# Performance work log

Hardware: AMD Instinct MI355X
Metric: run time of the kernel (lower is better)

Reference implementation:

```python
import jax, jax.numpy as jnp
from jax import lax
import numpy as np

CH = 16
STAGES = 6
DN = ('NDHWC', 'DHWIO', 'NDHWC')


def setup_inputs() -> dict:
    key = jax.random.key(0)
    ks = jax.random.split(key, 16)
    B, G = 8, 64
    x = jax.random.normal(ks[0], (B, G, G, G, 1), dtype=jnp.float32)
    mask = jax.random.randint(ks[1], (B, G, G, G), 0, 2, dtype=jnp.int32)
    meta = jax.random.normal(ks[2], (B, 3), dtype=jnp.float32)
    sched = jax.random.normal(ks[3], (B, 128), dtype=jnp.float32)
    s = 0.05
    w_stem = jax.random.normal(ks[4], (5, 5, 5, 1, CH), dtype=jnp.float32) * s
    w_stages = jax.random.normal(ks[5], (STAGES, 3, 3, 3, CH, CH), dtype=jnp.float32) * s
    meta_w1 = jax.random.normal(ks[6], (3, 32), dtype=jnp.float32) * s
    meta_b1 = jnp.zeros((32,), jnp.float32)
    meta_w2 = jax.random.normal(ks[7], (32, 16), dtype=jnp.float32) * s
    meta_b2 = jnp.zeros((16,), jnp.float32)
    mat_w = jax.random.normal(ks[8], (CH * STAGES + 16, 128), dtype=jnp.float32) * s
    mat_b = jnp.zeros((128,), jnp.float32)
    sch_w = jax.random.normal(ks[9], (128, 128), dtype=jnp.float32) * s
    sch_b = jnp.zeros((128,), jnp.float32)
    f1_w = jax.random.normal(ks[10], (256, 128), dtype=jnp.float32) * s
    f1_b = jnp.zeros((128,), jnp.float32)
    f2_w = jax.random.normal(ks[11], (128, 1), dtype=jnp.float32) * s
    f2_b = jnp.zeros((1,), jnp.float32)
    return dict(x=x, mask=mask, meta=meta, sched=sched, w_stem=w_stem,
                w_stages=w_stages, meta_w1=meta_w1, meta_b1=meta_b1,
                meta_w2=meta_w2, meta_b2=meta_b2, mat_w=mat_w, mat_b=mat_b,
                sch_w=sch_w, sch_b=sch_b, f1_w=f1_w, f1_b=f1_b,
                f2_w=f2_w, f2_b=f2_b)


def _pool_mask(m):
    # ME stride-2 output coords = unique(coords // 2): 2x2x2 max-pool, ceil sizes
    return lax.reduce_window(m, jnp.float32(0), lax.max,
                             (1, 2, 2, 2), (1, 2, 2, 2), 'SAME')


def reference(x, mask, meta, sched, w_stem, w_stages, meta_w1, meta_b1,
              meta_w2, meta_b2, mat_w, mat_b, sch_w, sch_b,
              f1_w, f1_b, f2_w, f2_b):
    m = mask.astype(x.dtype)
    feats = x * m[..., None]                       # zero features off-mask
    y = lax.conv_general_dilated(feats, w_stem, (1, 1, 1), 'SAME',
                                 dimension_numbers=DN)
    y = jnp.maximum(y * m[..., None], 0.0)         # stem: conv + mask + ReLU
    pools = []
    for i in range(STAGES):
        y = lax.conv_general_dilated(y, w_stages[i], (2, 2, 2),
                                     [(1, 1), (1, 1), (1, 1)],
                                     dimension_numbers=DN)
        m = _pool_mask(m)
        y = jnp.maximum(y * m[..., None], 0.0)
        denom = jnp.maximum(m.sum(axis=(1, 2, 3)), 1.0)   # occupied voxels
        pools.append(y.sum(axis=(1, 2, 3)) / denom[:, None])
    pools = jnp.concatenate(pools, axis=1)                 # [B, CH*STAGES]
    h = jax.nn.relu(meta[:, :3] @ meta_w1 + meta_b1)
    meta_emb = h @ meta_w2 + meta_b2                        # [B,16]
    m_emb = jax.nn.relu(jnp.concatenate([pools, meta_emb], 1) @ mat_w + mat_b)
    s_emb = jax.nn.relu(sched @ sch_w + sch_b)
    z = jnp.concatenate([m_emb, s_emb], axis=1)             # [B,256]
    z = jax.nn.relu(z @ f1_w + f1_b)
    return z @ f2_w + f2_b                                  # [B,1]
```

## Files before the change

### kernel.cpp

```cpp
#include <hip/hip_runtime.h>

#define CH 16
#define NB 8

typedef unsigned short u16;
typedef unsigned int u32;
typedef __attribute__((ext_vector_type(8))) short s16x8;
typedef __attribute__((ext_vector_type(4))) float f32x4;

__device__ __forceinline__ float bflo(u32 u) { return __uint_as_float(u << 16); }
__device__ __forceinline__ float bfhi(u32 u) { return __uint_as_float(u & 0xffff0000u); }
__device__ __forceinline__ u32 bfrnd(float f) {
  u32 u = __float_as_uint(f);
  return (u + 0x7fffu + ((u >> 16) & 1u)) >> 16;
}
__device__ __forceinline__ u32 packbf(float lo, float hi) {
  return bfrnd(lo) | (bfrnd(hi) << 16);
}

__global__ __launch_bounds__(256) void bprep_kernel(
    const float* __restrict__ w_stg, const float* __restrict__ w_stem,
    u16* __restrict__ bpre)
{
  const int e = blockIdx.x * 256 + (int)threadIdx.x;
  if (e >= 4 * 7168 + 3584) return;
  if (e < 4 * 7168) {
    const int s = e / 7168, r0 = e % 7168;
    const int i = r0 >> 9;
    const int r = r0 & 511;
    const int l = r >> 3, j = r & 7;
    const int tap = 2 * i + (l >> 5);
    const int cin = ((l >> 4) & 1) * 8 + j;
    const int n = l & 15;
    const float* w = w_stg + s * 27 * 256;
    const float val = (tap < 27) ? w[(tap * 16 + cin) * 16 + n] : 0.f;
    bpre[s * 7168 + i * 512 + l * 8 + j] = (u16)bfrnd(val);
  } else {
    const int e2 = e - 4 * 7168;
    const int i = e2 >> 9;
    const int r0 = e2 & 511;
    const int lane = r0 >> 3, j = r0 & 7;
    const int quad = lane >> 4, n = lane & 15;
    const int r = i * 4 + quad;
    const float val = (r < 25 && j < 5) ? w_stem[(r * 5 + j) * 16 + n] : 0.f;
    bpre[4 * 7168 + e2] = (u16)bfrnd(val);
  }
}

__global__ __launch_bounds__(256) void stem_mfma(
    const float* __restrict__ x, const int* __restrict__ mask,
    const u16* __restrict__ bpre, u16* __restrict__ yout,
    float* __restrict__ pool_sum, float* __restrict__ cnt)
{
  __shared__ u16 tl[144 * 24];
  __shared__ u16 cp[8 * 1168];

  const int b = blockIdx.y;
  const int u = blockIdx.x;
  const int tb = ((u & 7) << 6) | (u >> 3);
  const int z0 = (tb >> 6) * 8;
  const int y0 = ((tb >> 3) & 7) * 8;
  const int x0 = (tb & 7) * 8;
  const int tid = threadIdx.x;

  if (tb == 0) {
    if (tid < 96) pool_sum[b * 96 + tid] = 0.f;
    else if (tid < 102) cnt[b * 6 + (tid - 96)] = 0.f;
  }

  const int lane = tid & 63;
  const int wv = tid >> 6;
  const int n = lane & 15;
  const int quad = lane >> 4;
  const int vy = n >> 2, vx = n & 3;

  s16x8 wf[7];
  {
    const s16x8* wfp = (const s16x8*)(bpre + 4 * 7168);
#pragma unroll
    for (int i = 0; i < 7; ++i) wf[i] = wfp[i * 64 + lane];
  }

  for (int i = tid; i < 1728; i += 256) {
    const int row = i / 12;
    const int lx = i - row * 12;
    const int lz = row / 12;
    const int ly = row - lz * 12;
    const int gz = z0 + lz - 2, gy = y0 + ly - 2, gx = x0 + lx - 2;
    float v = 0.f;
    if ((unsigned)gz < 64u && (unsigned)gy < 64u && (unsigned)gx < 64u) {
      const int gi = ((b * 64 + gz) * 64 + gy) * 64 + gx;
      v = x[gi] * (float)mask[gi];
    }
    tl[row * 24 + lx] = (u16)bfrnd(v);
  }
  __syncthreads();

  if (tid < 144) {
    const uint4 a = *(const uint4*)&tl[tid * 24];
    const uint2 bq = *(const uint2*)&tl[tid * 24 + 8];
    u32 c[7];
    c[0] = a.x; c[1] = a.y; c[2] = a.z; c[3] = a.w;
    c[4] = bq.x; c[5] = bq.y; c[6] = 0u;
    u32 d[7];
#pragma unroll
    for (int k = 0; k < 6; ++k) d[k] = (c[k] >> 16) | (c[k + 1] << 16);
    d[6] = c[6] >> 16;
    uint4* dst = (uint4*)&cp[tid * 8];
    dst[0 * 146] = make_uint4(c[0], c[1], c[2], c[3]);
    dst[1 * 146] = make_uint4(d[0], d[1], d[2], d[3]);
    dst[2 * 146] = make_uint4(c[1], c[2], c[3], c[4]);
    dst[3 * 146] = make_uint4(d[1], d[2], d[3], d[4]);
    dst[4 * 146] = make_uint4(c[2], c[3], c[4], c[5]);
    dst[5 * 146] = make_uint4(d[2], d[3], d[4], d[5]);
    dst[6 * 146] = make_uint4(c[3], c[4], c[5], c[6]);
    dst[7 * 146] = make_uint4(d[3], d[4], d[5], d[6]);
  }
  __syncthreads();

  int doff[7];
#pragma unroll
  for (int i = 0; i < 7; ++i) {
    const int r = i * 4 + quad;
    doff[i] = (r < 25) ? ((r / 5) * 12 + (r % 5)) * 8 : 0;
  }

  for (int s = 0; s < 8; ++s) {
    const int sz = (s >> 2) * 4, sy = ((s >> 1) & 1) * 4, sx = (s & 1) * 4;
    const int base =
        (sx + vx) * 1168 + (((sz + wv) * 12) + (sy + vy)) * 8;
    f32x4 acc = {0.f, 0.f, 0.f, 0.f};
#pragma unroll
    for (int i = 0; i < 7; ++i) {
      const s16x8 bf = *(const s16x8*)&cp[base + doff[i]];
      acc = __builtin_amdgcn_mfma_f32_16x16x32_bf16(wf[i], bf, acc, 0, 0, 0);
    }
    const int Z = z0 + sz + wv, Y = y0 + sy + vy, X = x0 + sx + vx;
    const int gi = ((b * 64 + Z) * 64 + Y) * 64 + X;
    const float mv = (float)mask[gi];
    const float f0 = fmaxf(acc[0], 0.f) * mv;
    const float f1 = fmaxf(acc[1], 0.f) * mv;
    const float f2 = fmaxf(acc[2], 0.f) * mv;
    const float f3 = fmaxf(acc[3], 0.f) * mv;
    uint2* op = (uint2*)(yout + (size_t)gi * CH + quad * 4);
    op[0] = make_uint2(packbf(f0, f1), packbf(f2, f3));
  }
}

template <int S>
__global__ __launch_bounds__(256) void stage_mfma4(
    const u16* __restrict__ yin, const u16* __restrict__ bpre,
    const int* __restrict__ m_in_i, const float* __restrict__ m_in_f,
    u16* __restrict__ yout, float* __restrict__ m_out,
    float* __restrict__ pool_sum, float* __restrict__ cnt,
    const int stage)
{
  __shared__ u16 lb[14 * 512];
  __shared__ float lC[4 * 16 * 17];
  __shared__ float lmp[256];

  constexpr int So = S >> 1;
  constexpr int nvox = So * So * So;
  const int b = blockIdx.y;
  const int tid = threadIdx.x;
  const int vg0 = blockIdx.x * 256;

  {
    const uint4* src = (const uint4*)bpre;
    uint4* dst = (uint4*)lb;
    for (int e = tid; e < 896; e += 256) dst[e] = src[e];
  }

  {
    const int vox = vg0 + tid;
    const int oz = vox / (So * So);
    const int oy = (vox / So) % So;
    const int ox = vox % So;
    float mp = 0.f;
#pragma unroll
    for (int dz = 0; dz < 2; ++dz)
#pragma unroll
      for (int dy = 0; dy < 2; ++dy)
#pragma unroll
        for (int dx = 0; dx < 2; ++dx) {
          const int mi =
              ((b * S + 2 * oz + dz) * S + 2 * oy + dy) * S + 2 * ox + dx;
          const float mv = m_in_i ? (float)m_in_i[mi] : m_in_f[mi];
          mp = fmaxf(mp, mv);
        }
    lmp[tid] = mp;
  }
  __syncthreads();

  const int wv = tid >> 6;
  const int lane = tid & 63;
  const int m = lane & 15;
  const int quad = lane >> 4;
  const int qh = quad >> 1;
  const int qlo = quad & 1;

  int izb[4], iyb[4], ixb[4];
#pragma unroll
  for (int g = 0; g < 4; ++g) {
    const int vox = vg0 + wv * 64 + g * 16 + m;
    const int oz = vox / (So * So);
    const int oy = (vox / So) % So;
    const int ox = vox % So;
    izb[g] = 2 * oz - 1;
    iyb[g] = 2 * oy - 1;
    ixb[g] = 2 * ox - 1;
  }

  const s16x8* lbv = (const s16x8*)lb;
  f32x4 acc[4];
#pragma unroll
  for (int g = 0; g < 4; ++g) acc[g] = (f32x4){0.f, 0.f, 0.f, 0.f};

#pragma unroll
  for (int i = 0; i < 14; ++i) {
    const int t0 = 2 * i, t1 = 2 * i + 1;
    const int dz0 = t0 / 9, dy0 = (t0 / 3) % 3, dx0 = t0 % 3;
    const int dz1 = (t1 < 27) ? t1 / 9 : 1;
    const int dy1 = (t1 < 27) ? (t1 / 3) % 3 : 1;
    const int dx1 = (t1 < 27) ? t1 % 3 : 1;
    const int dzq = qh ? dz1 : dz0;
    const int dyq = qh ? dy1 : dy0;
    const int dxq = qh ? dx1 : dx0;

    uint4 ar[4];
#pragma unroll
    for (int g = 0; g < 4; ++g) {
      const int iz = izb[g] + dzq;
      const int iy = iyb[g] + dyq;
      const int ix = ixb[g] + dxq;
      const bool valid = (unsigned)iz < (unsigned)S &&
                         (unsigned)iy < (unsigned)S &&
                         (unsigned)ix < (unsigned)S;
      const int izc = min(max(iz, 0), S - 1);
      const int iyc = min(max(iy, 0), S - 1);
      const int ixc = min(max(ix, 0), S - 1);
      const size_t addr =
          (size_t)(((b * S + izc) * S + iyc) * S + ixc) * 16 + qlo * 8;
      uint4 v = *(const uint4*)(yin + addr);
      v.x = valid ? v.x : 0u;
      v.y = valid ? v.y : 0u;
      v.z = valid ? v.z : 0u;
      v.w = valid ? v.w : 0u;
      ar[g] = v;
    }
    const s16x8 bfrag = lbv[i * 64 + lane];
#pragma unroll
    for (int g = 0; g < 4; ++g)
      acc[g] = __builtin_amdgcn_mfma_f32_16x16x32_bf16(
          __builtin_bit_cast(s16x8, ar[g]), bfrag, acc[g], 0, 0, 0);
  }

  float psum = 0.f;
#pragma unroll
  for (int g = 0; g < 4; ++g) {
    __syncthreads();
    {
      float* lCw = lC + wv * 272;
      const int n = lane & 15;
#pragma unroll
      for (int reg = 0; reg < 4; ++reg) {
        const int row = quad * 4 + reg;
        lCw[row * 17 + n] =
            fmaxf(acc[g][reg], 0.f) * lmp[wv * 64 + g * 16 + row];
      }
    }
    __syncthreads();
    {
      const int vox_l = tid >> 2;
      const int cg = (tid & 3) * 4;
      const float* src = lC + (vox_l >> 4) * 272 + (vox_l & 15) * 17 + cg;
      const float f0 = src[0], f1 = src[1], f2 = src[2], f3 = src[3];
      const int lv = (vox_l >> 4) * 64 + g * 16 + (vox_l & 15);
      const size_t gi = (size_t)b * nvox + vg0 + lv;
      uint2* op = (uint2*)(yout + gi * 16 + cg);
      op[0] = make_uint2(packbf(f0, f1), packbf(f2, f3));
      if ((tid & 3) == 0) m_out[gi] = lmp[lv];
    }
    if (tid < 16) {
      float s = 0.f;
#pragma unroll 16
      for (int v = 0; v < 64; ++v)
        s += lC[(v >> 4) * 272 + (v & 15) * 17 + tid];
      psum += s;
    }
  }
  if (tid < 16) {
    atomicAdd(&pool_sum[(b * 6 + stage) * 16 + tid], psum);
  } else if (tid == 16) {
    float c = 0.f;
#pragma unroll 16
    for (int v = 0; v < 256; ++v) c += lmp[v];
    atomicAdd(&cnt[b * 6 + stage], c);
  }
}

__global__ __launch_bounds__(256) void tail_kernel(
    const u16* __restrict__ y3g, const float* __restrict__ m3g,
    const u16* __restrict__ bpre,
    const float* __restrict__ wstg,
    const float* __restrict__ meta, const float* __restrict__ sched,
    const float* __restrict__ mw1, const float* __restrict__ mb1,
    const float* __restrict__ mw2, const float* __restrict__ mb2,
    const float* __restrict__ matw, const float* __restrict__ matb,
    const float* __restrict__ schw, const float* __restrict__ schb,
    const float* __restrict__ f1w, const float* __restrict__ f1b,
    const float* __restrict__ f2w, const float* __restrict__ f2b,
    const float* __restrict__ pool_sum, const float* __restrict__ cnt,
    float* __restrict__ out)
{
  const int b = blockIdx.x;
  const int t = threadIdx.x;
  __shared__ u16 ty3[8192];
  __shared__ float lm3[512];
  __shared__ float pb[4 * 64 * 17];
  __shared__ float ly4[64 * 16];
  __shared__ float lm4[64];
  __shared__ float ps4[256];
  __shared__ float ly5[8 * 16];
  __shared__ float lm5[8];
  __shared__ float ps5[128];
  __shared__ float lsum[3][16];
  __shared__ float lcnt[3];
  __shared__ float invec[112];
  __shared__ float hbuf[32];
  __shared__ float zbuf[256];
  __shared__ float psf[256];
  __shared__ float part[2];

  {
    const uint4* yb = (const uint4*)(y3g + (size_t)b * 8192);
    uint4* dst = (uint4*)ty3;
    for (int i = t; i < 1024; i += 256) dst[i] = yb[i];
    for (int i = t; i < 512; i += 256) lm3[i] = m3g[b * 512 + i];
  }
  __syncthreads();

  {
    const int lane = t & 63;
    const int wv = t >> 6;
    const int mm = lane & 15;
    const int quad = lane >> 4;
    const int qh = quad >> 1, qlo = quad & 1;

    int iz0[4], iy0[4], ix0[4];
#pragma unroll
    for (int g = 0; g < 4; ++g) {
      const int vox = g * 16 + mm;
      iz0[g] = 2 * (vox >> 4) - 1;
      iy0[g] = 2 * ((vox >> 2) & 3) - 1;
      ix0[g] = 2 * (vox & 3) - 1;
    }
    f32x4 a3[4];
#pragma unroll
    for (int g = 0; g < 4; ++g) a3[g] = (f32x4){0.f, 0.f, 0.f, 0.f};
    const s16x8* bp3 = (const s16x8*)(bpre + 3 * 7168);
#pragma unroll
    for (int ii = 0; ii < 4; ++ii) {
      const int i = wv * 4 + ii;
      if (i < 14) {
        const int t0 = 2 * i, t1 = 2 * i + 1;
        const int dz0 = t0 / 9, dy0 = (t0 / 3) % 3, dx0 = t0 % 3;
        const int dz1 = (t1 < 27) ? t1 / 9 : 1;
        const int dy1 = (t1 < 27) ? (t1 / 3) % 3 : 1;
        const int dx1 = (t1 < 27) ? t1 % 3 : 1;
        const int dzq = qh ? dz1 : dz0;
        const int dyq = qh ? dy1 : dy0;
        const int dxq = qh ? dx1 : dx0;
        uint4 ar[4];
#pragma unroll
        for (int g = 0; g < 4; ++g) {
          const int iz = iz0[g] + dzq;
          const int iy = iy0[g] + dyq;
          const int ix = ix0[g] + dxq;
          const bool valid = (unsigned)iz < 8u && (unsigned)iy < 8u &&
                             (unsigned)ix < 8u;
          const int izc = min(max(iz, 0), 7);
          const int iyc = min(max(iy, 0), 7);
          const int ixc = min(max(ix, 0), 7);
          const int ad = ((izc * 8 + iyc) * 8 + ixc) * 16 + qlo * 8;
          uint4 v = *(const uint4*)&ty3[ad];
          v.x = valid ? v.x : 0u;
          v.y = valid ? v.y : 0u;
          v.z = valid ? v.z : 0u;
          v.w = valid ? v.w : 0u;
          ar[g] = v;
        }
        const s16x8 bf = bp3[i * 64 + lane];
#pragma unroll
        for (int g = 0; g < 4; ++g)
          a3[g] = __builtin_amdgcn_mfma_f32_16x16x32_bf16(
              __builtin_bit_cast(s16x8, ar[g]), bf, a3[g], 0, 0, 0);
      }
    }
#pragma unroll
    for (int g = 0; g < 4; ++g)
#pragma unroll
      for (int reg = 0; reg < 4; ++reg)
        pb[wv * 1088 + (g * 16 + quad * 4 + reg) * 17 + mm] = a3[g][reg];
  }
  __syncthreads();

  {
    const int vox = t >> 2, cg = (t & 3) * 4;
    const int oz = vox >> 4, oy = (vox >> 2) & 3, ox = vox & 3;
    float mp = 0.f;
#pragma unroll
    for (int dz = 0; dz < 2; ++dz)
#pragma unroll
      for (int dy = 0; dy < 2; ++dy)
#pragma unroll
        for (int dx = 0; dx < 2; ++dx)
          mp = fmaxf(mp, lm3[((2 * oz + dz) * 8 + 2 * oy + dy) * 8 +
                             2 * ox + dx]);
#pragma unroll
    for (int c = 0; c < 4; ++c) {
      const int ch = cg + c;
      const float s = pb[vox * 17 + ch] + pb[1088 + vox * 17 + ch] +
                      pb[2176 + vox * 17 + ch] + pb[3264 + vox * 17 + ch];
      ly4[vox * 16 + ch] = fmaxf(s, 0.f) * mp;
    }
    if (cg == 0) lm4[vox] = mp;
  }
  __syncthreads();

  if (t < 16) {
    float s = 0.f;
#pragma unroll 16
    for (int v = 0; v < 64; ++v) s += ly4[v * 16 + t];
    lsum[0][t] = s;
  } else if (t == 16) {
    float s = 0.f;
#pragma unroll 16
    for (int v = 0; v < 64; ++v) s += lm4[v];
    lcnt[0] = s;
  }
  {
    const float* w = wstg + 4 * 27 * 256;
    const int o = t >> 1, kh = t & 1;
    const int vox4 = o >> 4, co = o & 15;
    const int oz = vox4 >> 2, oy = (vox4 >> 1) & 1, ox = vox4 & 1;
    float acc = 0.f;
#pragma unroll
    for (int tt = 0; tt < 14; ++tt) {
      const int tap = tt + (kh ? 14 : 0);
      if (tap < 27) {
        const int dz = tap / 9, dy = (tap / 3) % 3, dx = tap % 3;
        const int iz = 2 * oz + dz - 1, iy = 2 * oy + dy - 1,
                  ix = 2 * ox + dx - 1;
        const float s = ((unsigned)iz < 4u && (unsigned)iy < 4u &&
                         (unsigned)ix < 4u) ? 1.f : 0.f;
        const int idx = ((min(max(iz, 0), 3) * 4 + min(max(iy, 0), 3)) * 4 +
                         min(max(ix, 0), 3)) * 16;
        const float* wp = w + tap * 256 + co;
#pragma unroll
        for (int ci = 0; ci < 16; ++ci)
          acc = fmaf(ly4[idx + ci] * s, wp[ci * 16], acc);
      }
    }
    ps4[t] = acc;
  }
  __syncthreads();

  if (t < 128) {
    const int vox4 = t >> 4, co = t & 15;
    float mp = 0.f;
#pragma unroll
    for (int dz = 0; dz < 2; ++dz)
#pragma unroll
      for (int dy = 0; dy < 2; ++dy)
#pragma unroll
        for (int dx = 0; dx < 2; ++dx)
          mp = fmaxf(mp, lm4[((2 * (vox4 >> 2) + dz) * 4 +
                              2 * ((vox4 >> 1) & 1) + dy) * 4 +
                             2 * (vox4 & 1) + dx]);
    ly5[t] = fmaxf(ps4[2 * t] + ps4[2 * t + 1], 0.f) * mp;
    if (co == 0) lm5[vox4] = mp;
  }
  __syncthreads();

  if (t < 16) {
    float s = 0.f;
#pragma unroll
    for (int v = 0; v < 8; ++v) s += ly5[v * 16 + t];
    lsum[1][t] = s;
  } else if (t == 16) {
    lcnt[1] = lm5[0] + lm5[1] + lm5[2] + lm5[3] + lm5[4] + lm5[5] + lm5[6] +
              lm5[7];
  }
  if (t < 128) {
    const float* w = wstg + 5 * 27 * 256;
    const int co = t & 15, k8 = t >> 4;
    float acc = 0.f;
#pragma unroll
    for (int tt = 0; tt < 4; ++tt) {
      const int tap = k8 * 4 + tt;
      if (tap < 27) {
        const int dz = tap / 9, dy = (tap / 3) % 3, dx = tap % 3;
        const int iz = dz - 1, iy = dy - 1, ix = dx - 1;
        const float s = ((unsigned)iz < 2u && (unsigned)iy < 2u &&
                         (unsigned)ix < 2u) ? 1.f : 0.f;
        const int idx = ((min(max(iz, 0), 1) * 2 + min(max(iy, 0), 1)) * 2 +
                         min(max(ix, 0), 1)) * 16;
        const float* wp = w + tap * 256 + co;
#pragma unroll
        for (int ci = 0; ci < 16; ++ci)
          acc = fmaf(ly5[idx + ci] * s, wp[ci * 16], acc);
      }
    }
    ps5[t] = acc;
  }
  __syncthreads();

  if (t < 16) {
    float s = ps5[t] + ps5[16 + t] + ps5[32 + t] + ps5[48 + t] +
              ps5[64 + t] + ps5[80 + t] + ps5[96 + t] + ps5[112 + t];
    float mp = 0.f;
#pragma unroll
    for (int v = 0; v < 8; ++v) mp = fmaxf(mp, lm5[v]);
    lsum[2][t] = fmaxf(s, 0.f) * mp;
    if (t == 0) lcnt[2] = mp;
  } else if (t >= 96 && t < 128) {
    const int j = t - 96;
    float h = mb1[j];
#pragma unroll
    for (int k = 0; k < 3; ++k) h = fmaf(meta[b * 3 + k], mw1[k * 32 + j], h);
    hbuf[j] = fmaxf(h, 0.f);
  }
  __syncthreads();

  if (t < 48) {
    const int s = t >> 4;
    invec[t] = pool_sum[b * 96 + t] / fmaxf(cnt[b * 6 + s], 1.f);
  } else if (t < 96) {
    const int s = (t >> 4) - 3;
    invec[t] = lsum[s][t & 15] / fmaxf(lcnt[s], 1.f);
  } else if (t < 112) {
    const int j = t - 96;
    float e = mb2[j];
#pragma unroll
    for (int k = 0; k < 32; ++k) e = fmaf(hbuf[k], mw2[k * 16 + j], e);
    invec[t] = e;
  }
  __syncthreads();

  if (t < 128) {
    float a = matb[t];
#pragma unroll 16
    for (int k = 0; k < 112; ++k) a = fmaf(invec[k], matw[k * 128 + t], a);
    zbuf[t] = fmaxf(a, 0.f);
  } else {
    const int c = t - 128;
    float s = schb[c];
#pragma unroll 16
    for (int k = 0; k < 128; ++k)
      s = fmaf(sched[b * 128 + k], schw[k * 128 + c], s);
    zbuf[128 + c] = fmaxf(s, 0.f);
  }
  __syncthreads();

  {
    const int col = t & 127, kh = t >> 7;
    float a = 0.f;
#pragma unroll 16
    for (int kk = 0; kk < 128; ++kk) {
      const int k = kh * 128 + kk;
      a = fmaf(zbuf[k], f1w[k * 128 + col], a);
    }
    psf[t] = a;
  }
  __syncthreads();

  if (t < 128) {
    const float a = psf[t] + psf[128 + t] + f1b[t];
    float v = fmaxf(a, 0.f) * f2w[t];
#pragma unroll
    for (int off = 32; off > 0; off >>= 1) v += __shfl_xor(v, off, 64);
    if ((t & 63) == 0) part[t >> 6] = v;
  }
  __syncthreads();
  if (t == 0) out[b] = part[0] + part[1] + f2b[0];
}

extern "C" void kernel_launch(void* const* d_in, const int* in_sizes, int n_in,
                              void* d_out, int out_size, void* d_ws,
                              size_t ws_size, hipStream_t stream)
{
  (void)in_sizes; (void)n_in; (void)out_size; (void)ws_size;
  const float* x      = (const float*)d_in[0];
  const int*   mask   = (const int*)  d_in[1];
  const float* meta   = (const float*)d_in[2];
  const float* sched  = (const float*)d_in[3];
  const float* w_stem = (const float*)d_in[4];
  const float* w_stg  = (const float*)d_in[5];
  const float* mw1    = (const float*)d_in[6];
  const float* mb1    = (const float*)d_in[7];
  const float* mw2    = (const float*)d_in[8];
  const float* mb2    = (const float*)d_in[9];
  const float* matw   = (const float*)d_in[10];
  const float* matb   = (const float*)d_in[11];
  const float* schw   = (const float*)d_in[12];
  const float* schb   = (const float*)d_in[13];
  const float* f1w    = (const float*)d_in[14];
  const float* f1b    = (const float*)d_in[15];
  const float* f2w    = (const float*)d_in[16];
  const float* f2b    = (const float*)d_in[17];
  float* out = (float*)d_out;

  char* ws = (char*)d_ws;
  size_t off = 0;
  auto alloc = [&](size_t nbytes) -> void* {
    void* p = ws + off;
    off += (nbytes + 255) & ~(size_t)255;
    return p;
  };

  u16* y0 = (u16*)alloc((size_t)NB * 64 * 64 * 64 * CH * 2);
  u16* y1 = (u16*)alloc((size_t)NB * 32 * 32 * 32 * CH * 2);
  u16* y2 = (u16*)alloc((size_t)NB * 16 * 16 * 16 * CH * 2);
  u16* y3 = (u16*)alloc((size_t)NB * 8 * 8 * 8 * CH * 2);
  float* m1 = (float*)alloc((size_t)NB * 32 * 32 * 32 * 4);
  float* m2 = (float*)alloc((size_t)NB * 16 * 16 * 16 * 4);
  float* m3 = (float*)alloc((size_t)NB * 8 * 8 * 8 * 4);
  float* pool_sum = (float*)alloc((NB * 96 + NB * 6) * 4);
  float* cnt = pool_sum + NB * 96;
  u16* bpre = (u16*)alloc((4 * 7168 + 3584) * 2);

  bprep_kernel<<<126, 256, 0, stream>>>(w_stg, w_stem, bpre);

  stem_mfma<<<dim3(512, NB), 256, 0, stream>>>(x, mask, bpre, y0,
                                               pool_sum, cnt);

  stage_mfma4<64><<<dim3(128, NB), 256, 0, stream>>>(
      y0, bpre + 0 * 7168, mask, (const float*)nullptr, y1, m1,
      pool_sum, cnt, 0);
  stage_mfma4<32><<<dim3(16, NB), 256, 0, stream>>>(
      y1, bpre + 1 * 7168, (const int*)nullptr, m1, y2, m2,
      pool_sum, cnt, 1);
  stage_mfma4<16><<<dim3(2, NB), 256, 0, stream>>>(
      y2, bpre + 2 * 7168, (const int*)nullptr, m2, y3, m3,
      pool_sum, cnt, 2);

  tail_kernel<<<NB, 256, 0, stream>>>(y3, m3, bpre, w_stg, meta, sched,
                                      mw1, mb1, mw2, mb2, matw, matb,
                                      schw, schb, f1w, f1b, f2w, f2b,
                                      pool_sum, cnt, out);
}
```

Before: 203.8 us.

## Fuse stem input staging into direct vectorized row loads with hardware bf16 packing

The stem kernel no longer stages the masked input tile into an intermediate LDS buffer. Each of 144 threads now loads its 12-element x row and mask row with float2/int2 vector loads and builds the shifted bf16 pairs directly in registers. This removes one LDS pass and one barrier. The output mask value is prefetched one sub-block ahead, output addresses are precomputed, a v_cvt_pk_bf16_f32 instruction replaces the software bf16 round-and-pack, and an occupancy hint of 6 is added to launch bounds. Fewer threads now participate in the global loads, so latency hiding during the load phase may be reduced.

Measured after the change: 196.5 us. 1.04x faster.

```diff
diff --git a/kernel.cpp b/kernel.cpp
--- a/kernel.cpp
+++ b/kernel.cpp
@@ -14,8 +14,10 @@
   u32 u = __float_as_uint(f);
   return (u + 0x7fffu + ((u >> 16) & 1u)) >> 16;
 }
-__device__ __forceinline__ u32 packbf(float lo, float hi) {
-  return bfrnd(lo) | (bfrnd(hi) << 16);
+__device__ __forceinline__ u32 packbf_hw(float lo, float hi) {
+  u32 r;
+  asm("v_cvt_pk_bf16_f32 %0, %1, %2" : "=v"(r) : "v"(lo), "v"(hi));
+  return r;
 }
 
 __global__ __launch_bounds__(256) void bprep_kernel(
@@ -47,12 +49,11 @@
   }
 }
 
-__global__ __launch_bounds__(256) void stem_mfma(
+__global__ __launch_bounds__(256, 6) void stem_mfma(
     const float* __restrict__ x, const int* __restrict__ mask,
     const u16* __restrict__ bpre, u16* __restrict__ yout,
     float* __restrict__ pool_sum, float* __restrict__ cnt)
 {
-  __shared__ u16 tl[144 * 24];
   __shared__ u16 cp[8 * 1168];
 
   const int b = blockIdx.y;
@@ -81,40 +82,63 @@
     for (int i = 0; i < 7; ++i) wf[i] = wfp[i * 64 + lane];
   }
 
-  for (int i = tid; i < 1728; i += 256) {
-    const int row = i / 12;
-    const int lx = i - row * 12;
-    const int lz = row / 12;
-    const int ly = row - lz * 12;
-    const int gz = z0 + lz - 2, gy = y0 + ly - 2, gx = x0 + lx - 2;
-    float v = 0.f;
-    if ((unsigned)gz < 64u && (unsigned)gy < 64u && (unsigned)gx < 64u) {
-      const int gi = ((b * 64 + gz) * 64 + gy) * 64 + gx;
-      v = x[gi] * (float)mask[gi];
-    }
-    tl[row * 24 + lx] = (u16)bfrnd(v);
-  }
-  __syncthreads();
-
   if (tid < 144) {
-    const uint4 a = *(const uint4*)&tl[tid * 24];
-    const uint2 bq = *(const uint2*)&tl[tid * 24 + 8];
-    u32 c[7];
-    c[0] = a.x; c[1] = a.y; c[2] = a.z; c[3] = a.w;
-    c[4] = bq.x; c[5] = bq.y; c[6] = 0u;
-    u32 d[7];
-#pragma unroll
-    for (int k = 0; k < 6; ++k) d[k] = (c[k] >> 16) | (c[k + 1] << 16);
-    d[6] = c[6] >> 16;
+    const int lz = tid / 12, ly = tid - lz * 12;
+    const int gz = z0 + lz - 2, gy = y0 + ly - 2;
     uint4* dst = (uint4*)&cp[tid * 8];
-    dst[0 * 146] = make_uint4(c[0], c[1], c[2], c[3]);
-    dst[1 * 146] = make_uint4(d[0], d[1], d[2], d[3]);
-    dst[2 * 146] = make_uint4(c[1], c[2], c[3], c[4]);
-    dst[3 * 146] = make_uint4(d[1], d[2], d[3], d[4]);
-    dst[4 * 146] = make_uint4(c[2], c[3], c[4], c[5]);
-    dst[5 * 146] = make_uint4(d[2], d[3], d[4], d[5]);
-    dst[6 * 146] = make_uint4(c[3], c[4], c[5], c[6]);
-    dst[7 * 146] = make_uint4(d[3], d[4], d[5], d[6]);
+    if ((unsigned)gz < 64u && (unsigned)gy < 64u) {
+      const long long rowg =
+          ((long long)((b * 64 + gz) * 64 + gy)) * 64 + (x0 - 2);
+      float v[12];
+      if (rowg >= 0 && rowg + 12 <= (long long)NB * 64 * 64 * 64) {
+        const float2* xp = (const float2*)(x + rowg);
+        const int2* mp2 = (const int2*)(mask + rowg);
+        float2 xv[6]; int2 mv2[6];
+#pragma unroll
+        for (int j = 0; j < 6; ++j) { xv[j] = xp[j]; mv2[j] = mp2[j]; }
+#pragma unroll
+        for (int j = 0; j < 6; ++j) {
+          v[2 * j]     = xv[j].x * (float)mv2[j].x;
+          v[2 * j + 1] = xv[j].y * (float)mv2[j].y;
+        }
+        if (x0 == 0)  { v[0] = 0.f;  v[1] = 0.f;  }
+        if (x0 == 56) { v[10] = 0.f; v[11] = 0.f; }
+      } else {
+#pragma unroll
+        for (int j = 0; j < 12; ++j) {
+          const int gx = x0 - 2 + j;
+          float vv = 0.f;
+          if ((unsigned)gx < 64u) {
+            const long long gi = rowg + j;
+            vv = x[gi] * (float)mask[gi];
+          }
+          v[j] = vv;
+        }
+      }
+      const u32 c0 = packbf_hw(v[0], v[1]);
+      const u32 c1 = packbf_hw(v[2], v[3]);
+      const u32 c2 = packbf_hw(v[4], v[5]);
+      const u32 c3 = packbf_hw(v[6], v[7]);
+      const u32 c4 = packbf_hw(v[8], v[9]);
+      const u32 c5 = packbf_hw(v[10], v[11]);
+      const u32 d0 = packbf_hw(v[1], v[2]);
+      const u32 d1 = packbf_hw(v[3], v[4]);
+      const u32 d2 = packbf_hw(v[5], v[6]);
+      const u32 d3 = packbf_hw(v[7], v[8]);
+      const u32 d4 = packbf_hw(v[9], v[10]);
+      const u32 d5 = packbf_hw(v[11], 0.f);
+      dst[0 * 146] = make_uint4(c0, c1, c2, c3);
+      dst[1 * 146] = make_uint4(d0, d1, d2, d3);
+      dst[2 * 146] = make_uint4(c1, c2, c3, c4);
+      dst[3 * 146] = make_uint4(d1, d2, d3, d4);
+      dst[4 * 146] = make_uint4(c2, c3, c4, c5);
+      dst[5 * 146] = make_uint4(d2, d3, d4, d5);
+      dst[6 * 146] = make_uint4(c3, c4, c5, 0u);
+      dst[7 * 146] = make_uint4(d3, d4, d5, 0u);
+    } else {
+#pragma unroll
+      for (int p = 0; p < 8; ++p) dst[p * 146] = make_uint4(0u, 0u, 0u, 0u);
+    }
   }
   __syncthreads();
 
@@ -124,26 +148,35 @@
     const int r = i * 4 + quad;
     doff[i] = (r < 25) ? ((r / 5) * 12 + (r % 5)) * 8 : 0;
   }
-
+  const int base0 = vx * 1168 + (wv * 12 + vy) * 8;
+  const int gi0 = ((b * 64 + z0 + wv) * 64 + y0 + vy) * 64 + x0 + vx;
+  u16* outp = yout + (size_t)gi0 * 16 + quad * 4;
+
+  float mvc = (float)mask[gi0];
   for (int s = 0; s < 8; ++s) {
-    const int sz = (s >> 2) * 4, sy = ((s >> 1) & 1) * 4, sx = (s & 1) * 4;
-    const int base =
-        (sx + vx) * 1168 + (((sz + wv) * 12) + (sy + vy)) * 8;
+    const int sz = (s >> 2) * 4, sy2 = ((s >> 1) & 1) * 4, sx = (s & 1) * 4;
+    const int off = sz * 4096 + sy2 * 64 + sx;
+    float mvn = 0.f;
+    if (s < 7) {
+      const int s1 = s + 1;
+      const int offn = ((s1 >> 2) * 4) * 4096 + (((s1 >> 1) & 1) * 4) * 64 +
+                       (s1 & 1) * 4;
+      mvn = (float)mask[gi0 + offn];
+    }
+    const int base = base0 + sx * 1168 + (sz * 12 + sy2) * 8;
     f32x4 acc = {0.f, 0.f, 0.f, 0.f};
 #pragma unroll
     for (int i = 0; i < 7; ++i) {
       const s16x8 bf = *(const s16x8*)&cp[base + doff[i]];
       acc = __builtin_amdgcn_mfma_f32_16x16x32_bf16(wf[i], bf, acc, 0, 0, 0);
     }
-    const int Z = z0 + sz + wv, Y = y0 + sy + vy, X = x0 + sx + vx;
-    const int gi = ((b * 64 + Z) * 64 + Y) * 64 + X;
-    const float mv = (float)mask[gi];
-    const float f0 = fmaxf(acc[0], 0.f) * mv;
-    const float f1 = fmaxf(acc[1], 0.f) * mv;
-    const float f2 = fmaxf(acc[2], 0.f) * mv;
-    const float f3 = fmaxf(acc[3], 0.f) * mv;
-    uint2* op = (uint2*)(yout + (size_t)gi * CH + quad * 4);
-    op[0] = make_uint2(packbf(f0, f1), packbf(f2, f3));
+    const float f0 = fmaxf(acc[0], 0.f) * mvc;
+    const float f1 = fmaxf(acc[1], 0.f) * mvc;
+    const float f2 = fmaxf(acc[2], 0.f) * mvc;
+    const float f3 = fmaxf(acc[3], 0.f) * mvc;
+    *(uint2*)(outp + (size_t)off * 16) =
+        make_uint2(packbf_hw(f0, f1), packbf_hw(f2, f3));
+    mvc = mvn;
   }
 }
 
@@ -278,7 +311,7 @@
       const int lv = (vox_l >> 4) * 64 + g * 16 + (vox_l & 15);
       const size_t gi = (size_t)b * nvox + vg0 + lv;
       uint2* op = (uint2*)(yout + gi * 16 + cg);
-      op[0] = make_uint2(packbf(f0, f1), packbf(f2, f3));
+      op[0] = make_uint2(packbf_hw(f0, f1), packbf_hw(f2, f3));
       if ((tid & 3) == 0) m_out[gi] = lmp[lv];
     }
     if (tid < 16) {
```
